# Kernel tuning notes

Measured on AMD Instinct MI355X. Metric: run time of the kernel, lower is better.

The kernel has to match this reference:

```python
import jax, jax.numpy as jnp
import numpy as np
import math

B, C, T, V = 64, 256, 120, 25
HEADS = 8


def entmax15(x, axis=-1):
    """Exact entmax with alpha=1.5 via the sort-based algorithm (Peters & Martins).
    Assumes axis=-1."""
    x = x / 2.0
    x = x - jnp.max(x, axis=axis, keepdims=True)
    xs = jnp.flip(jnp.sort(x, axis=axis), axis=axis)  # descending
    n = x.shape[axis]
    k = jnp.arange(1, n + 1, dtype=x.dtype)
    cum = jnp.cumsum(xs, axis=-1)
    mean = cum / k
    ss = jnp.cumsum(xs * xs, axis=-1) - cum * mean  # k * (mean_sq - mean^2)
    delta = (1.0 - ss) / k
    tau = mean - jnp.sqrt(jnp.maximum(delta, 0.0))
    support = jnp.sum((tau <= xs).astype(jnp.int32), axis=-1, keepdims=True)
    tau_star = jnp.take_along_axis(tau, support - 1, axis=-1)
    return jnp.maximum(x - tau_star, 0.0) ** 2


def setup_inputs() -> dict:
    key = jax.random.key(0)
    ks = jax.random.split(key, 10)
    s = 1.0 / math.sqrt(C)  # torch Linear default init scale
    return {
        "x": jax.random.normal(ks[0], (B, C, T, V), dtype=jnp.float32),
        "y": jax.random.normal(ks[1], (B, C, T), dtype=jnp.float32),
        "Wq": jax.random.uniform(ks[2], (C, C), jnp.float32, -s, s),
        "bq": jax.random.uniform(ks[3], (C,), jnp.float32, -s, s),
        "Wk": jax.random.uniform(ks[4], (C, C), jnp.float32, -s, s),
        "bk": jax.random.uniform(ks[5], (C,), jnp.float32, -s, s),
        "Wv": jax.random.uniform(ks[6], (C, C), jnp.float32, -s, s),
        "bv": jax.random.uniform(ks[7], (C,), jnp.float32, -s, s),
        "Wo": jax.random.uniform(ks[8], (C, C), jnp.float32, -s, s),
        "bo": jax.random.uniform(ks[9], (C,), jnp.float32, -s, s),
    }


def reference(x, y, Wq, bq, Wk, bk, Wv, bv, Wo, bo):
    Bx, Cx, Tx, Vx = x.shape
    H = HEADS
    Dh = Cx // H
    BT = Bx * Tx
    # p: [B*T, V, C]; y -> [B*T, 1, C]
    p = jnp.transpose(x, (0, 2, 3, 1)).reshape(BT, Vx, Cx)
    ykv = jnp.transpose(y, (0, 2, 1)).reshape(BT, 1, Cx)
    q = (p @ Wq.T + bq).reshape(BT, Vx, H, Dh).transpose(0, 2, 1, 3)   # [BT,H,V,Dh]
    k = (ykv @ Wk.T + bk).reshape(BT, 1, H, Dh).transpose(0, 2, 1, 3)  # [BT,H,1,Dh]
    v = (ykv @ Wv.T + bv).reshape(BT, 1, H, Dh).transpose(0, 2, 1, 3)  # [BT,H,1,Dh]
    scores = jnp.einsum('bhqd,bhkd->bhqk', q, k) / math.sqrt(Dh)       # [BT,H,V,1]
    attn = entmax15(scores, axis=-1)
    out = jnp.einsum('bhqk,bhkd->bhqd', attn, v)                        # [BT,H,V,Dh]
    out = out.transpose(0, 2, 1, 3).reshape(BT, Vx, Cx)
    out = out @ Wo.T + bo
    z = out.reshape(Bx, Tx, Vx, Cx).transpose(0, 3, 1, 2) + x          # [B,C,T,V]
    return z
```

## Files before the change

kernel.cpp:

```cpp
#include <hip/hip_runtime.h>
#include <cstddef>

#define B_DIM 64
#define C_DIM 256
#define T_DIM 120
#define V_DIM 25
#define TV    3000
#define CTILE 16

typedef float f4v __attribute__((ext_vector_type(4)));

__global__ __launch_bounds__(256) void make_wc(
    const float* __restrict__ Wo, const float* __restrict__ Wv,
    const float* __restrict__ bv, const float* __restrict__ bo,
    float* __restrict__ WcT, float* __restrict__ bc) {
  const int c = blockIdx.x;
  const int i = threadIdx.x;

  float acc = 0.0f;
#pragma unroll 8
  for (int j = 0; j < C_DIM; ++j) {
    acc = fmaf(Wo[c * C_DIM + j], Wv[j * C_DIM + i], acc);
  }
  WcT[i * C_DIM + c] = acc;

  __shared__ float red[C_DIM];
  red[i] = Wo[c * C_DIM + i] * bv[i];
  __syncthreads();
  for (int s = 128; s > 0; s >>= 1) {
    if (i < s) red[i] += red[i + s];
    __syncthreads();
  }
  if (i == 0) bc[c] = red[0] + bo[c];
}

__global__ __launch_bounds__(256) void ov_kernel(
    const float* __restrict__ y, const float* __restrict__ WcT,
    const float* __restrict__ bc, float* __restrict__ ov) {
  const int b   = blockIdx.x;
  const int c0  = blockIdx.y * CTILE;
  const int tid = threadIdx.x;
  const int chalf = tid >> 7;
  const int t     = tid & 127;
  if (t >= T_DIM) return;

  const int cb = __builtin_amdgcn_readfirstlane(c0 + chalf * 8);

  float acc[8];
#pragma unroll
  for (int cl = 0; cl < 8; ++cl) acc[cl] = bc[cb + cl];

  const float* yb = y + (size_t)b * C_DIM * T_DIM + t;

  for (int i = 0; i < C_DIM; i += 8) {
    float yv[8];
#pragma unroll
    for (int u = 0; u < 8; ++u) yv[u] = yb[(size_t)(i + u) * T_DIM];
#pragma unroll
    for (int u = 0; u < 8; ++u) {
      const f4v* wr = (const f4v*)(WcT + (i + u) * C_DIM + cb);
      const f4v w0 = wr[0];
      const f4v w1 = wr[1];
      acc[0] = fmaf(w0.x, yv[u], acc[0]);
      acc[1] = fmaf(w0.y, yv[u], acc[1]);
      acc[2] = fmaf(w0.z, yv[u], acc[2]);
      acc[3] = fmaf(w0.w, yv[u], acc[3]);
      acc[4] = fmaf(w1.x, yv[u], acc[4]);
      acc[5] = fmaf(w1.y, yv[u], acc[5]);
      acc[6] = fmaf(w1.z, yv[u], acc[6]);
      acc[7] = fmaf(w1.w, yv[u], acc[7]);
    }
  }

  float* ovp = ov + ((size_t)b * C_DIM + cb) * T_DIM + t;
#pragma unroll
  for (int cl = 0; cl < 8; ++cl) ovp[(size_t)cl * T_DIM] = acc[cl];
}

__global__ __launch_bounds__(256) void add_kernel(
    const float* __restrict__ x, const float* __restrict__ ov,
    float* __restrict__ z) {
  const int NF4    = B_DIM * C_DIM * TV / 4;
  const int stride = gridDim.x * 256;
  const f4v* __restrict__ xin  = (const f4v*)x;
  f4v* __restrict__       zout = (f4v*)z;

  for (int idx = blockIdx.x * 256 + threadIdx.x; idx < NF4; idx += stride) {
    const int pos    = idx * 4;
    const int row    = pos / TV;
    const int within = pos - row * TV;
    const int t0     = within / V_DIM;
    const int r      = within - t0 * V_DIM;

    const float* ovr = ov + (size_t)row * T_DIM;
    const float a0 = ovr[t0];
    const int   t1 = (t0 < T_DIM - 1) ? (t0 + 1) : t0;
    const float a1 = ovr[t1];

    f4v xv = __builtin_nontemporal_load(&xin[idx]);
    f4v o;
    o.x = xv.x + a0;
    o.y = xv.y + ((r + 1 < V_DIM) ? a0 : a1);
    o.z = xv.z + ((r + 2 < V_DIM) ? a0 : a1);
    o.w = xv.w + ((r + 3 < V_DIM) ? a0 : a1);
    __builtin_nontemporal_store(o, &zout[idx]);
  }
}

extern "C" void kernel_launch(void* const* d_in, const int* in_sizes, int n_in,
                              void* d_out, int out_size, void* d_ws, size_t ws_size,
                              hipStream_t stream) {
  const float* x  = (const float*)d_in[0];
  const float* y  = (const float*)d_in[1];
  const float* Wv = (const float*)d_in[6];
  const float* bv = (const float*)d_in[7];
  const float* Wo = (const float*)d_in[8];
  const float* bo = (const float*)d_in[9];
  float* z = (float*)d_out;

  float* ov  = (float*)d_ws;
  float* WcT = ov + (size_t)B_DIM * C_DIM * T_DIM;
  float* bc  = WcT + C_DIM * C_DIM;

  make_wc<<<dim3(C_DIM), dim3(C_DIM), 0, stream>>>(Wo, Wv, bv, bo, WcT, bc);

  ov_kernel<<<dim3(B_DIM, C_DIM / CTILE), dim3(256), 0, stream>>>(y, WcT, bc, ov);

  add_kernel<<<dim3(2048), dim3(256), 0, stream>>>(x, ov, z);
}
```

Baseline: 111.9 us.

## Tile add kernel per (batch, channel tile) and stage ov rows in shared memory

The broadcast-add kernel now gives each block one batch and a 16-channel tile. The block first copies that tile's ov rows into LDS, then streams the contiguous x slab and adds values read from LDS. This replaces the global gathers of ov and the 64-bit-free divisions by TV in a grid-stride loop. It also drops the nontemporal load/store hints in favour of plain vector accesses, which may change cache behaviour for this streaming-bound kernel.

```diff
diff --git a/kernel.cpp b/kernel.cpp
--- a/kernel.cpp
+++ b/kernel.cpp
@@ -80,30 +80,43 @@
 __global__ __launch_bounds__(256) void add_kernel(
     const float* __restrict__ x, const float* __restrict__ ov,
     float* __restrict__ z) {
-  const int NF4    = B_DIM * C_DIM * TV / 4;
-  const int stride = gridDim.x * 256;
-  const f4v* __restrict__ xin  = (const f4v*)x;
-  f4v* __restrict__       zout = (f4v*)z;
+  const int b   = blockIdx.x;
+  const int c0  = blockIdx.y * CTILE;
+  const int tid = threadIdx.x;
 
-  for (int idx = blockIdx.x * 256 + threadIdx.x; idx < NF4; idx += stride) {
-    const int pos    = idx * 4;
-    const int row    = pos / TV;
-    const int within = pos - row * TV;
-    const int t0     = within / V_DIM;
-    const int r      = within - t0 * V_DIM;
+  __shared__ float ovl[CTILE * T_DIM + 4];
 
-    const float* ovr = ov + (size_t)row * T_DIM;
-    const float a0 = ovr[t0];
-    const int   t1 = (t0 < T_DIM - 1) ? (t0 + 1) : t0;
-    const float a1 = ovr[t1];
+  {
+    const f4v* __restrict__ src =
+        (const f4v*)(ov + ((size_t)b * C_DIM + c0) * T_DIM);
+    f4v* dst = (f4v*)ovl;
+    for (int i = tid; i < (CTILE * T_DIM) / 4; i += 256) dst[i] = src[i];
+  }
+  __syncthreads();
 
-    f4v xv = __builtin_nontemporal_load(&xin[idx]);
+  const size_t base = ((size_t)b * C_DIM + c0) * TV;
+  const f4v* __restrict__ xin  = (const f4v*)(x + base);
+  f4v* __restrict__       zout = (f4v*)(z + base);
+  const int nf4 = CTILE * TV / 4;
+
+  for (int idx = tid; idx < nf4; idx += 256) {
+    const int cl  = idx / 750;
+    const int p4  = idx - cl * 750;
+    const int pos = p4 * 4;
+    const int t0  = pos / 25;
+    const int r   = pos - t0 * 25;
+
+    const float* row = ovl + cl * T_DIM;
+    const float a0 = row[t0];
+    const float a1 = row[t0 + 1];
+
+    const f4v xv = xin[idx];
     f4v o;
     o.x = xv.x + a0;
     o.y = xv.y + ((r + 1 < V_DIM) ? a0 : a1);
     o.z = xv.z + ((r + 2 < V_DIM) ? a0 : a1);
     o.w = xv.w + ((r + 3 < V_DIM) ? a0 : a1);
-    __builtin_nontemporal_store(o, &zout[idx]);
+    zout[idx] = o;
   }
 }
 
@@ -126,5 +139,5 @@
 
   ov_kernel<<<dim3(B_DIM, C_DIM / CTILE), dim3(256), 0, stream>>>(y, WcT, bc, ov);
 
-  add_kernel<<<dim3(2048), dim3(256), 0, stream>>>(x, ov, z);
+  add_kernel<<<dim3(B_DIM, C_DIM / CTILE), dim3(256), 0, stream>>>(x, ov, z);
 }
```

Measured after the change: 124.8 us. 11.6% more time.
